# Optimization experiments

Measured on AMD Instinct MI355X. Metric: run time of the kernel, lower is better.

Reference implementation:

```python
import jax, jax.numpy as jnp
import numpy as np

B, N, D, H = 64, 4096, 128, 256


def setup_inputs() -> dict:
    key = jax.random.key(0)
    k1, k2, k3 = jax.random.split(key, 3)
    feats = jax.random.normal(k1, (B, N, D), dtype=jnp.float32)
    # Linear init scale ~ 1/sqrt(fan_in) to keep scores well-conditioned
    W1 = jax.random.normal(k2, (D, H), dtype=jnp.float32) / np.sqrt(D)
    b1 = jnp.zeros((H,), dtype=jnp.float32)
    W2 = jax.random.normal(k3, (H, 1), dtype=jnp.float32) / np.sqrt(H)
    b2 = jnp.zeros((1,), dtype=jnp.float32)
    return {"feats": feats, "W1": W1, "b1": b1, "W2": W2, "b2": b2}


def reference(feats, W1, b1, W2, b2):
    # scalar attention score per node: fc = Linear -> ReLU -> Linear(->1)
    h = jax.nn.relu(jnp.einsum('bnd,dh->bnh', feats, W1) + b1)  # [B,N,H]
    scores = jnp.einsum('bnh,ho->bno', h, W2) + b2              # [B,N,1]
    w = jax.nn.softmax(scores, axis=1)                          # softmax over nodes
    out = jnp.sum(w * feats, axis=1)                            # [B,D]
    return out
```

## Files before the change

### kernel.cpp

```cpp
#include <hip/hip_runtime.h>
#include <math.h>

#define BB 64
#define NN 4096
#define DD 128
#define HH 256
#define MB 256
#define NBLK (BB * NN / MB)
#define PSTRIDE 132

typedef __attribute__((ext_vector_type(8))) _Float16 f16x8;
typedef __attribute__((ext_vector_type(4))) float f32x4;

static __device__ __forceinline__ void gload_lds16(const void* g, void* l) {
    __builtin_amdgcn_global_load_lds(
        (const __attribute__((address_space(1))) unsigned int*)g,
        (__attribute__((address_space(3))) unsigned int*)l, 16, 0, 0);
}

__global__ __launch_bounds__(256) void k_prep(const float* __restrict__ W1,
                                              char* __restrict__ Bws) {
    const int k = blockIdx.x;
    const int c = threadIdx.x;
    const _Float16 h = (_Float16)W1[k * HH + c];
    const int chunk = c >> 4, cl = c & 15;
    const int off = ((cl << 8) + (k << 1)) ^ ((cl & 7) << 4);
    *(_Float16*)(Bws + chunk * 4096 + off) = h;
}

__global__ __launch_bounds__(256, 2) void k_fused(const float* __restrict__ feats,
                                                  const char* __restrict__ Bws,
                                                  const float* __restrict__ b1,
                                                  const float* __restrict__ W2,
                                                  float* __restrict__ parts) {
    __shared__ char  Bl[65536];
    __shared__ float scores_l[256];
    __shared__ float ew[256];
    __shared__ float wacc[4][128];
    __shared__ float redm[4], redz[4];

    const int tid  = threadIdx.x;
    const int lane = tid & 63;
    const int wv   = tid >> 6;
    const int blk  = blockIdx.x;
    const int rl   = lane & 15;
    const int q    = lane >> 4;

    #pragma unroll
    for (int it = 0; it < 16; ++it)
        gload_lds16(Bws + it * 4096 + tid * 16, Bl + it * 4096 + tid * 16);

    f16x8 af[4][4];
    const float* fbase = feats + (size_t)blk * MB * DD;
    #pragma unroll
    for (int t = 0; t < 4; ++t) {
        const float* rp = fbase + (wv * 64 + t * 16 + rl) * DD + q * 8;
        #pragma unroll
        for (int kk = 0; kk < 4; ++kk) {
            float4 v0 = *(const float4*)(rp + kk * 32);
            float4 v1 = *(const float4*)(rp + kk * 32 + 4);
            f16x8 a;
            a[0] = (_Float16)v0.x; a[1] = (_Float16)v0.y;
            a[2] = (_Float16)v0.z; a[3] = (_Float16)v0.w;
            a[4] = (_Float16)v1.x; a[5] = (_Float16)v1.y;
            a[6] = (_Float16)v1.z; a[7] = (_Float16)v1.w;
            af[t][kk] = a;
        }
    }
    __syncthreads();

    float sp[4][4] = {{0,0,0,0},{0,0,0,0},{0,0,0,0},{0,0,0,0}};
    const int brow = rl << 8;
    const int bswz = (rl & 7) << 4;
    const int bq   = q << 4;

    for (int chunk = 0; chunk < 16; ++chunk) {
        const float bbv = b1[chunk * 16 + rl];
        const float ww  = W2[chunk * 16 + rl];
        const char* cb = Bl + chunk * 4096;
        f32x4 acc0 = {0,0,0,0}, acc1 = {0,0,0,0}, acc2 = {0,0,0,0}, acc3 = {0,0,0,0};
        #pragma unroll
        for (int kk = 0; kk < 4; ++kk) {
            f16x8 bf = *(const f16x8*)(cb + (((brow + (kk << 6) + bq)) ^ bswz));
            acc0 = __builtin_amdgcn_mfma_f32_16x16x32_f16(af[0][kk], bf, acc0, 0, 0, 0);
            acc1 = __builtin_amdgcn_mfma_f32_16x16x32_f16(af[1][kk], bf, acc1, 0, 0, 0);
            acc2 = __builtin_amdgcn_mfma_f32_16x16x32_f16(af[2][kk], bf, acc2, 0, 0, 0);
            acc3 = __builtin_amdgcn_mfma_f32_16x16x32_f16(af[3][kk], bf, acc3, 0, 0, 0);
        }
        #pragma unroll
        for (int j = 0; j < 4; ++j) {
            sp[0][j] += fmaxf(acc0[j] + bbv, 0.f) * ww;
            sp[1][j] += fmaxf(acc1[j] + bbv, 0.f) * ww;
            sp[2][j] += fmaxf(acc2[j] + bbv, 0.f) * ww;
            sp[3][j] += fmaxf(acc3[j] + bbv, 0.f) * ww;
        }
    }

    #pragma unroll
    for (int m = 1; m < 16; m <<= 1)
        #pragma unroll
        for (int t = 0; t < 4; ++t)
            #pragma unroll
            for (int j = 0; j < 4; ++j)
                sp[t][j] += __shfl_xor(sp[t][j], m);
    if (rl == 0) {
        #pragma unroll
        for (int t = 0; t < 4; ++t)
            #pragma unroll
            for (int j = 0; j < 4; ++j)
                scores_l[wv * 64 + t * 16 + q * 4 + j] = sp[t][j];
    }
    __syncthreads();

    const float s = scores_l[tid];
    float mx = s;
    #pragma unroll
    for (int o = 1; o < 64; o <<= 1) mx = fmaxf(mx, __shfl_xor(mx, o));
    if (lane == 0) redm[wv] = mx;
    __syncthreads();
    mx = fmaxf(fmaxf(redm[0], redm[1]), fmaxf(redm[2], redm[3]));
    const float e = expf(s - mx);
    ew[tid] = e;
    float z = e;
    #pragma unroll
    for (int o = 1; o < 64; o <<= 1) z += __shfl_xor(z, o);
    if (lane == 0) redz[wv] = z;
    __syncthreads();
    const float zblk = redz[0] + redz[1] + redz[2] + redz[3];

    const float w0 = ew[wv * 64 +  0 + rl];
    const float w1 = ew[wv * 64 + 16 + rl];
    const float w2 = ew[wv * 64 + 32 + rl];
    const float w3 = ew[wv * 64 + 48 + rl];
    float acc[4][8];
    #pragma unroll
    for (int kk = 0; kk < 4; ++kk)
        #pragma unroll
        for (int e8 = 0; e8 < 8; ++e8)
            acc[kk][e8] = w0 * (float)af[0][kk][e8] + w1 * (float)af[1][kk][e8]
                        + w2 * (float)af[2][kk][e8] + w3 * (float)af[3][kk][e8];
    #pragma unroll
    for (int m = 1; m < 16; m <<= 1)
        #pragma unroll
        for (int kk = 0; kk < 4; ++kk)
            #pragma unroll
            for (int e8 = 0; e8 < 8; ++e8)
                acc[kk][e8] += __shfl_xor(acc[kk][e8], m);
    if (rl == 0) {
        #pragma unroll
        for (int kk = 0; kk < 4; ++kk)
            #pragma unroll
            for (int e8 = 0; e8 < 8; ++e8)
                wacc[wv][kk * 32 + q * 8 + e8] = acc[kk][e8];
    }
    __syncthreads();

    if (tid < 128) {
        float p = wacc[0][tid] + wacc[1][tid] + wacc[2][tid] + wacc[3][tid];
        parts[blk * PSTRIDE + tid] = p;
    } else if (tid == 128) {
        parts[blk * PSTRIDE + 128] = mx;
        parts[blk * PSTRIDE + 129] = zblk;
    }
}

__global__ __launch_bounds__(128) void k_out(const float* __restrict__ parts,
                                             float* __restrict__ out) {
    const int b = blockIdx.x;
    const int d = threadIdx.x;
    const float* pb = parts + (size_t)b * 16 * PSTRIDE;
    float M = -1e30f;
    #pragma unroll
    for (int i = 0; i < 16; ++i) M = fmaxf(M, pb[i * PSTRIDE + 128]);
    float num = 0.f, den = 0.f;
    #pragma unroll
    for (int i = 0; i < 16; ++i) {
        const float sc = expf(pb[i * PSTRIDE + 128] - M);
        num = fmaf(sc, pb[i * PSTRIDE + d], num);
        den = fmaf(sc, pb[i * PSTRIDE + 129], den);
    }
    out[b * DD + d] = num / den;
}

extern "C" void kernel_launch(void* const* d_in, const int* in_sizes, int n_in,
                              void* d_out, int out_size, void* d_ws, size_t ws_size,
                              hipStream_t stream) {
    const float* feats = (const float*)d_in[0];
    const float* W1    = (const float*)d_in[1];
    const float* b1    = (const float*)d_in[2];
    const float* W2    = (const float*)d_in[3];
    float* out = (float*)d_out;

    char*  Bws   = (char*)d_ws;
    float* parts = (float*)((char*)d_ws + 65536);

    hipLaunchKernelGGL(k_prep, dim3(DD), dim3(HH), 0, stream, W1, Bws);
    hipLaunchKernelGGL(k_fused, dim3(NBLK), dim3(256), 0, stream,
                       feats, Bws, b1, W2, parts);
    hipLaunchKernelGGL(k_out, dim3(BB), dim3(128), 0, stream, parts, out);
}
```

Measured before the change: 54.45 us.

## Process two tiles per block with per-wave online softmax to amortize W1 LDS load

Each block now covers 512 nodes instead of 256, and each wave loops over two 64-row tiles. An online softmax (running max and rescaled sum) is kept per wave, so block-level shared-memory reductions and barriers are no longer needed. Each wave writes its own partial, so the final kernel merges 32 partials per batch instead of 16. The aim is to halve the number of times the 64KB W1 copy is loaded into LDS and to drop synchronization. In exchange there are half as many blocks (512), which lowers parallelism, the tile loop serializes its loads, and the online softmax adds extra exp and rescale work.

```diff
diff --git a/kernel.cpp b/kernel.cpp
--- a/kernel.cpp
+++ b/kernel.cpp
@@ -5,8 +5,7 @@
 #define NN 4096
 #define DD 128
 #define HH 256
-#define MB 256
-#define NBLK (BB * NN / MB)
+#define PPB 32
 #define PSTRIDE 132
 
 typedef __attribute__((ext_vector_type(8))) _Float16 f16x8;
@@ -33,134 +32,142 @@
                                                   const float* __restrict__ b1,
                                                   const float* __restrict__ W2,
                                                   float* __restrict__ parts) {
-    __shared__ char  Bl[65536];
-    __shared__ float scores_l[256];
-    __shared__ float ew[256];
-    __shared__ float wacc[4][128];
-    __shared__ float redm[4], redz[4];
-
-    const int tid  = threadIdx.x;
-    const int lane = tid & 63;
-    const int wv   = tid >> 6;
-    const int blk  = blockIdx.x;
-    const int rl   = lane & 15;
-    const int q    = lane >> 4;
+    __shared__ char Bl[65536];
+
+    const int tid   = threadIdx.x;
+    const int lane  = tid & 63;
+    const int wv    = tid >> 6;
+    const int batch = blockIdx.x >> 3;
+    const int slice = blockIdx.x & 7;
+    const int rl    = lane & 15;
+    const int q     = lane >> 4;
 
     #pragma unroll
     for (int it = 0; it < 16; ++it)
         gload_lds16(Bws + it * 4096 + tid * 16, Bl + it * 4096 + tid * 16);
-
-    f16x8 af[4][4];
-    const float* fbase = feats + (size_t)blk * MB * DD;
-    #pragma unroll
-    for (int t = 0; t < 4; ++t) {
-        const float* rp = fbase + (wv * 64 + t * 16 + rl) * DD + q * 8;
-        #pragma unroll
-        for (int kk = 0; kk < 4; ++kk) {
-            float4 v0 = *(const float4*)(rp + kk * 32);
-            float4 v1 = *(const float4*)(rp + kk * 32 + 4);
-            f16x8 a;
-            a[0] = (_Float16)v0.x; a[1] = (_Float16)v0.y;
-            a[2] = (_Float16)v0.z; a[3] = (_Float16)v0.w;
-            a[4] = (_Float16)v1.x; a[5] = (_Float16)v1.y;
-            a[6] = (_Float16)v1.z; a[7] = (_Float16)v1.w;
-            af[t][kk] = a;
-        }
-    }
     __syncthreads();
 
-    float sp[4][4] = {{0,0,0,0},{0,0,0,0},{0,0,0,0},{0,0,0,0}};
     const int brow = rl << 8;
     const int bswz = (rl & 7) << 4;
     const int bq   = q << 4;
 
-    for (int chunk = 0; chunk < 16; ++chunk) {
-        const float bbv = b1[chunk * 16 + rl];
-        const float ww  = W2[chunk * 16 + rl];
-        const char* cb = Bl + chunk * 4096;
-        f32x4 acc0 = {0,0,0,0}, acc1 = {0,0,0,0}, acc2 = {0,0,0,0}, acc3 = {0,0,0,0};
-        #pragma unroll
-        for (int kk = 0; kk < 4; ++kk) {
-            f16x8 bf = *(const f16x8*)(cb + (((brow + (kk << 6) + bq)) ^ bswz));
-            acc0 = __builtin_amdgcn_mfma_f32_16x16x32_f16(af[0][kk], bf, acc0, 0, 0, 0);
-            acc1 = __builtin_amdgcn_mfma_f32_16x16x32_f16(af[1][kk], bf, acc1, 0, 0, 0);
-            acc2 = __builtin_amdgcn_mfma_f32_16x16x32_f16(af[2][kk], bf, acc2, 0, 0, 0);
-            acc3 = __builtin_amdgcn_mfma_f32_16x16x32_f16(af[3][kk], bf, acc3, 0, 0, 0);
+    float m = -1e30f, z = 0.f;
+    float acc[4][8] = {{0,0,0,0,0,0,0,0},{0,0,0,0,0,0,0,0},
+                       {0,0,0,0,0,0,0,0},{0,0,0,0,0,0,0,0}};
+    const float* fb = feats + ((size_t)batch * NN + slice * 512 + wv * 128) * DD;
+
+    for (int tile = 0; tile < 2; ++tile) {
+        f16x8 af[4][4];
+        #pragma unroll
+        for (int t = 0; t < 4; ++t) {
+            const float* rp = fb + (tile * 64 + t * 16 + rl) * DD + q * 8;
+            #pragma unroll
+            for (int kk = 0; kk < 4; ++kk) {
+                float4 v0 = *(const float4*)(rp + kk * 32);
+                float4 v1 = *(const float4*)(rp + kk * 32 + 4);
+                f16x8 a;
+                a[0] = (_Float16)v0.x; a[1] = (_Float16)v0.y;
+                a[2] = (_Float16)v0.z; a[3] = (_Float16)v0.w;
+                a[4] = (_Float16)v1.x; a[5] = (_Float16)v1.y;
+                a[6] = (_Float16)v1.z; a[7] = (_Float16)v1.w;
+                af[t][kk] = a;
+            }
         }
-        #pragma unroll
-        for (int j = 0; j < 4; ++j) {
-            sp[0][j] += fmaxf(acc0[j] + bbv, 0.f) * ww;
-            sp[1][j] += fmaxf(acc1[j] + bbv, 0.f) * ww;
-            sp[2][j] += fmaxf(acc2[j] + bbv, 0.f) * ww;
-            sp[3][j] += fmaxf(acc3[j] + bbv, 0.f) * ww;
+
+        float sp[4][4] = {{0,0,0,0},{0,0,0,0},{0,0,0,0},{0,0,0,0}};
+        #pragma unroll
+        for (int chunk = 0; chunk < 16; ++chunk) {
+            const float bbv = b1[chunk * 16 + rl];
+            const float ww  = W2[chunk * 16 + rl];
+            const char* cb = Bl + chunk * 4096;
+            f32x4 a0 = {0,0,0,0}, a1 = {0,0,0,0}, a2 = {0,0,0,0}, a3 = {0,0,0,0};
+            #pragma unroll
+            for (int kk = 0; kk < 4; ++kk) {
+                f16x8 bf = *(const f16x8*)(cb + ((brow + (kk << 6) + bq) ^ bswz));
+                a0 = __builtin_amdgcn_mfma_f32_16x16x32_f16(af[0][kk], bf, a0, 0, 0, 0);
+                a1 = __builtin_amdgcn_mfma_f32_16x16x32_f16(af[1][kk], bf, a1, 0, 0, 0);
+                a2 = __builtin_amdgcn_mfma_f32_16x16x32_f16(af[2][kk], bf, a2, 0, 0, 0);
+                a3 = __builtin_amdgcn_mfma_f32_16x16x32_f16(af[3][kk], bf, a3, 0, 0, 0);
+            }
+            #pragma unroll
+            for (int j = 0; j < 4; ++j) {
+                sp[0][j] += fmaxf(a0[j] + bbv, 0.f) * ww;
+                sp[1][j] += fmaxf(a1[j] + bbv, 0.f) * ww;
+                sp[2][j] += fmaxf(a2[j] + bbv, 0.f) * ww;
+                sp[3][j] += fmaxf(a3[j] + bbv, 0.f) * ww;
+            }
         }
-    }
-
-    #pragma unroll
-    for (int m = 1; m < 16; m <<= 1)
+        #pragma unroll
+        for (int o = 1; o < 16; o <<= 1)
+            #pragma unroll
+            for (int t = 0; t < 4; ++t)
+                #pragma unroll
+                for (int j = 0; j < 4; ++j)
+                    sp[t][j] += __shfl_xor(sp[t][j], o);
+
+        float mt = sp[0][0];
         #pragma unroll
         for (int t = 0; t < 4; ++t)
             #pragma unroll
             for (int j = 0; j < 4; ++j)
-                sp[t][j] += __shfl_xor(sp[t][j], m);
+                mt = fmaxf(mt, sp[t][j]);
+        mt = fmaxf(mt, __shfl_xor(mt, 16));
+        mt = fmaxf(mt, __shfl_xor(mt, 32));
+        const float mnew  = fmaxf(m, mt);
+        const float scale = expf(m - mnew);
+        float ze = 0.f;
+        #pragma unroll
+        for (int t = 0; t < 4; ++t)
+            #pragma unroll
+            for (int j = 0; j < 4; ++j) {
+                sp[t][j] = expf(sp[t][j] - mnew);
+                ze += sp[t][j];
+            }
+        ze += __shfl_xor(ze, 16);
+        ze += __shfl_xor(ze, 32);
+        z = z * scale + ze;
+        m = mnew;
+        #pragma unroll
+        for (int kk = 0; kk < 4; ++kk)
+            #pragma unroll
+            for (int e8 = 0; e8 < 8; ++e8)
+                acc[kk][e8] *= scale;
+
+        const int srcl = (rl >> 2) << 4;
+        const int jsel = rl & 3;
+        #pragma unroll
+        for (int t = 0; t < 4; ++t) {
+            const float c0 = __shfl(sp[t][0], srcl);
+            const float c1 = __shfl(sp[t][1], srcl);
+            const float c2 = __shfl(sp[t][2], srcl);
+            const float c3 = __shfl(sp[t][3], srcl);
+            const float et = jsel == 0 ? c0 : jsel == 1 ? c1 : jsel == 2 ? c2 : c3;
+            #pragma unroll
+            for (int kk = 0; kk < 4; ++kk)
+                #pragma unroll
+                for (int e8 = 0; e8 < 8; ++e8)
+                    acc[kk][e8] = fmaf(et, (float)af[t][kk][e8], acc[kk][e8]);
+        }
+    }
+
+    #pragma unroll
+    for (int o = 1; o < 16; o <<= 1)
+        #pragma unroll
+        for (int kk = 0; kk < 4; ++kk)
+            #pragma unroll
+            for (int e8 = 0; e8 < 8; ++e8)
+                acc[kk][e8] += __shfl_xor(acc[kk][e8], o);
+    const int pbase = (batch * PPB + slice * 4 + wv) * PSTRIDE;
     if (rl == 0) {
         #pragma unroll
-        for (int t = 0; t < 4; ++t)
-            #pragma unroll
-            for (int j = 0; j < 4; ++j)
-                scores_l[wv * 64 + t * 16 + q * 4 + j] = sp[t][j];
-    }
-    __syncthreads();
-
-    const float s = scores_l[tid];
-    float mx = s;
-    #pragma unroll
-    for (int o = 1; o < 64; o <<= 1) mx = fmaxf(mx, __shfl_xor(mx, o));
-    if (lane == 0) redm[wv] = mx;
-    __syncthreads();
-    mx = fmaxf(fmaxf(redm[0], redm[1]), fmaxf(redm[2], redm[3]));
-    const float e = expf(s - mx);
-    ew[tid] = e;
-    float z = e;
-    #pragma unroll
-    for (int o = 1; o < 64; o <<= 1) z += __shfl_xor(z, o);
-    if (lane == 0) redz[wv] = z;
-    __syncthreads();
-    const float zblk = redz[0] + redz[1] + redz[2] + redz[3];
-
-    const float w0 = ew[wv * 64 +  0 + rl];
-    const float w1 = ew[wv * 64 + 16 + rl];
-    const float w2 = ew[wv * 64 + 32 + rl];
-    const float w3 = ew[wv * 64 + 48 + rl];
-    float acc[4][8];
-    #pragma unroll
-    for (int kk = 0; kk < 4; ++kk)
-        #pragma unroll
-        for (int e8 = 0; e8 < 8; ++e8)
-            acc[kk][e8] = w0 * (float)af[0][kk][e8] + w1 * (float)af[1][kk][e8]
-                        + w2 * (float)af[2][kk][e8] + w3 * (float)af[3][kk][e8];
-    #pragma unroll
-    for (int m = 1; m < 16; m <<= 1)
-        #pragma unroll
         for (int kk = 0; kk < 4; ++kk)
             #pragma unroll
             for (int e8 = 0; e8 < 8; ++e8)
-                acc[kk][e8] += __shfl_xor(acc[kk][e8], m);
-    if (rl == 0) {
-        #pragma unroll
-        for (int kk = 0; kk < 4; ++kk)
-            #pragma unroll
-            for (int e8 = 0; e8 < 8; ++e8)
-                wacc[wv][kk * 32 + q * 8 + e8] = acc[kk][e8];
-    }
-    __syncthreads();
-
-    if (tid < 128) {
-        float p = wacc[0][tid] + wacc[1][tid] + wacc[2][tid] + wacc[3][tid];
-        parts[blk * PSTRIDE + tid] = p;
-    } else if (tid == 128) {
-        parts[blk * PSTRIDE + 128] = mx;
-        parts[blk * PSTRIDE + 129] = zblk;
+                parts[pbase + kk * 32 + q * 8 + e8] = acc[kk][e8];
+    }
+    if (lane == 0) {
+        parts[pbase + 128] = m;
+        parts[pbase + 129] = z;
     }
 }
 
@@ -168,13 +175,13 @@
                                              float* __restrict__ out) {
     const int b = blockIdx.x;
     const int d = threadIdx.x;
-    const float* pb = parts + (size_t)b * 16 * PSTRIDE;
+    const float* pb = parts + (size_t)b * PPB * PSTRIDE;
     float M = -1e30f;
     #pragma unroll
-    for (int i = 0; i < 16; ++i) M = fmaxf(M, pb[i * PSTRIDE + 128]);
+    for (int i = 0; i < PPB; ++i) M = fmaxf(M, pb[i * PSTRIDE + 128]);
     float num = 0.f, den = 0.f;
     #pragma unroll
-    for (int i = 0; i < 16; ++i) {
+    for (int i = 0; i < PPB; ++i) {
         const float sc = expf(pb[i * PSTRIDE + 128] - M);
         num = fmaf(sc, pb[i * PSTRIDE + d], num);
         den = fmaf(sc, pb[i * PSTRIDE + 129], den);
@@ -195,7 +202,7 @@
     float* parts = (float*)((char*)d_ws + 65536);
 
     hipLaunchKernelGGL(k_prep, dim3(DD), dim3(HH), 0, stream, W1, Bws);
-    hipLaunchKernelGGL(k_fused, dim3(NBLK), dim3(256), 0, stream,
+    hipLaunchKernelGGL(k_fused, dim3(BB * 8), dim3(256), 0, stream,
                        feats, Bws, b1, W2, parts);
     hipLaunchKernelGGL(k_out, dim3(BB), dim3(128), 0, stream, parts, out);
 }
```

Measured after the change: 94.59 us. 73.7% more time.
